# Performance work log

Hardware: AMD Instinct MI355X
Metric: run time of the kernel (lower is better)

## Reference

```python
import jax, jax.numpy as jnp
import numpy as np

N_NODES = 50000
N_PATHS = 4
N_EDGES = 800000
D_IN = 256
D_OUT = 256
D_HID = 128  # SemanticAttention default hidden_size


def setup_inputs() -> dict:
    key = jax.random.key(0)
    ks = jax.random.split(key, 6)
    x = jax.random.normal(ks[0], (N_NODES, D_IN), dtype=jnp.float32)
    edge_indices = jax.random.randint(ks[1], (N_PATHS, 2, N_EDGES), 0, N_NODES)
    Ws = jax.random.normal(ks[2], (N_PATHS, D_IN, D_OUT), dtype=jnp.float32) * (1.0 / np.sqrt(D_IN))
    bs = jnp.zeros((N_PATHS, D_OUT), dtype=jnp.float32)
    attn_w1 = jax.random.normal(ks[3], (D_OUT, D_HID), dtype=jnp.float32) * (1.0 / np.sqrt(D_OUT))
    attn_b1 = jnp.zeros((D_HID,), dtype=jnp.float32)
    attn_w2 = jax.random.normal(ks[4], (D_HID, 1), dtype=jnp.float32) * (1.0 / np.sqrt(D_HID))
    return {"x": x, "edge_indices": edge_indices, "Ws": Ws, "bs": bs,
            "attn_w1": attn_w1, "attn_b1": attn_b1, "attn_w2": attn_w2}


def _gcn_conv(x, W, b, edges):
    """PyG GCNConv with normalize=True, add_self_loops=True.
    out = D^{-1/2} (A + I) D^{-1/2} (x @ W) + b
    """
    n = x.shape[0]
    xw = x @ W  # [N, D_OUT]
    loop = jnp.arange(n, dtype=edges.dtype)
    src = jnp.concatenate([edges[0], loop])
    dst = jnp.concatenate([edges[1], loop])
    ones = jnp.ones(src.shape[0], dtype=x.dtype)
    deg = jax.ops.segment_sum(ones, dst, num_segments=n)  # in-degree incl. self loop
    dinv = jnp.where(deg > 0, jax.lax.rsqrt(deg), 0.0)
    norm = dinv[src] * dinv[dst]  # [E+N]
    msgs = xw[src] * norm[:, None]  # gather + scale
    return jax.ops.segment_sum(msgs, dst, num_segments=n) + b  # scatter-add


def reference(x, edge_indices, Ws, bs, attn_w1, attn_b1, attn_w2):
    P = edge_indices.shape[0]
    # per-meta-path GCN embeddings, stacked -> [N, P, D_OUT]
    z = jnp.stack([_gcn_conv(x, Ws[i], bs[i], edge_indices[i]) for i in range(P)], axis=1)
    # semantic attention: per-node softmax over meta-paths
    w = jnp.tanh(z @ attn_w1 + attn_b1) @ attn_w2  # [N, P, 1]
    beta = jax.nn.softmax(w, axis=1)
    return (beta * z).sum(axis=1)  # [N, D_OUT]
```

## Files before the change

kernel.cpp:

```cpp
#include <hip/hip_runtime.h>
#include <hip/hip_fp16.h>
#include <cstdint>
#include <cstddef>

#define NN 50000
#define NE 800000
#define NP 4
#define DD 256
#define HH 128
#define MPAD 50048
#define PADIDX 50000

#define NB 196
#define CAP 5120
#define SCAP 6144
#define EPB 4096
#define NBB ((NE + EPB - 1) / EPB)
#define BIN_BLOCKS (NBB * NP)

typedef _Float16 f16x8 __attribute__((ext_vector_type(8)));
typedef float f32x4 __attribute__((ext_vector_type(4)));
typedef unsigned short u16x8 __attribute__((ext_vector_type(8)));
typedef unsigned short u16x4 __attribute__((ext_vector_type(4)));

#define X_OCT (NN * DD / 8)
#define XP_OCT (MPAD * DD / 8)
#define W_OCT (NP * DD * DD / 8)
#define W1_OCT (HH * DD / 8)
#define CVT_BLOCKS ((XP_OCT + W_OCT + W1_OCT + 255) / 256)
#define GEMM_BLOCKS ((MPAD / 64) * NP)

__global__ __launch_bounds__(256) void k_bin(const int* __restrict__ edges,
                                             int* __restrict__ gcnt,
                                             unsigned int* __restrict__ binned,
                                             const float* __restrict__ x,
                                             const float* __restrict__ Ws,
                                             const float* __restrict__ w1,
                                             _Float16* __restrict__ xh,
                                             _Float16* __restrict__ Wt,
                                             _Float16* __restrict__ w1t) {
    const int bx = blockIdx.x;
    const int tid = threadIdx.x;
    if (bx < BIN_BLOCKS) {
        __shared__ int hist[256], lb[256], cur[256], gbase[256], wsum[4];
        __shared__ unsigned int stage[EPB];
        const int p  = bx / NBB;
        const int bc = bx - p * NBB;
        const int e0 = bc * EPB;
        const int total = min(EPB, NE - e0);
        const int* es = edges + (size_t)p * 2 * NE;
        const int* ed = es + NE;
        hist[tid] = 0;
        __syncthreads();
        unsigned int word[16];
        int bkt[16];
#pragma unroll
        for (int j = 0; j < 16; j++) {
            int e = e0 + j * 256 + tid;
            bkt[j] = -1;
            if (e < NE) {
                int dst = ed[e];
                int src = es[e];
                int b = dst >> 8;
                bkt[j] = b;
                word[j] = ((unsigned)b << 24) | ((unsigned)(dst & 255) << 16) | (unsigned)src;
                atomicAdd(&hist[b], 1);
            }
        }
        __syncthreads();
        const int lane = tid & 63, wv = tid >> 6;
        int v = hist[tid];
        int incl = v;
#pragma unroll
        for (int off = 1; off < 64; off <<= 1) {
            int u = __shfl_up(incl, off);
            if (lane >= off) incl += u;
        }
        if (lane == 63) wsum[wv] = incl;
        __syncthreads();
        int wbase = 0;
        for (int i = 0; i < wv; i++) wbase += wsum[i];
        int excl = wbase + incl - v;
        lb[tid] = excl;
        cur[tid] = excl;
        if (tid < NB && v > 0) gbase[tid] = atomicAdd(&gcnt[p * NB + tid], v);
        __syncthreads();
#pragma unroll
        for (int j = 0; j < 16; j++)
            if (bkt[j] >= 0) {
                int r = atomicAdd(&cur[bkt[j]], 1);
                stage[r] = word[j];
            }
        __syncthreads();
        for (int s = tid; s < total; s += 256) {
            unsigned int wd = stage[s];
            int b = wd >> 24;
            int posl = gbase[b] + (s - lb[b]);
            if (posl < CAP)
                binned[(size_t)(p * NB + b) * CAP + posl] = wd & 0x00FFFFFFu;
        }
        return;
    }
    int i = (bx - BIN_BLOCKS) * 256 + tid;
    if (i < XP_OCT) {
        f16x8 o;
        if (i < X_OCT) {
            const float4* src = (const float4*)x + (size_t)i * 2;
            float4 v0 = src[0], v1 = src[1];
            o[0] = (_Float16)v0.x; o[1] = (_Float16)v0.y; o[2] = (_Float16)v0.z; o[3] = (_Float16)v0.w;
            o[4] = (_Float16)v1.x; o[5] = (_Float16)v1.y; o[6] = (_Float16)v1.z; o[7] = (_Float16)v1.w;
        } else {
#pragma unroll
            for (int t = 0; t < 8; t++) o[t] = (_Float16)0.0f;
        }
        *((f16x8*)xh + i) = o;
    } else if (i < XP_OCT + W_OCT) {
        int j = i - XP_OCT;
        int p   = j / (DD * DD / 8);
        int rem = j - p * (DD * DD / 8);
        int n   = rem >> 5;
        int k8  = (rem & 31) * 8;
        const float* wp = Ws + (size_t)p * DD * DD;
        f16x8 o;
#pragma unroll
        for (int t = 0; t < 8; t++) o[t] = (_Float16)wp[(size_t)(k8 + t) * DD + n];
        *((f16x8*)(Wt + (size_t)p * DD * DD + (size_t)n * DD + k8)) = o;
    } else if (i < XP_OCT + W_OCT + W1_OCT) {
        int j = i - XP_OCT - W_OCT;
        int n  = j >> 5;
        int k8 = (j & 31) * 8;
        f16x8 o;
#pragma unroll
        for (int t = 0; t < 8; t++) o[t] = (_Float16)w1[(size_t)(k8 + t) * HH + n];
        *((f16x8*)(w1t + (size_t)n * DD + k8)) = o;
    }
}

__global__ __launch_bounds__(256) void k_sort(const int* __restrict__ gcnt,
                                              const unsigned int* __restrict__ binned,
                                              unsigned short* __restrict__ srcs,
                                              int* __restrict__ offs,
                                              int* __restrict__ ends,
                                              float* __restrict__ dinv) {
    __shared__ int hist[256], cur[256], wsum[4];
    __shared__ unsigned short sorted[SCAP];
    const int bx = blockIdx.x;
    const int tid = threadIdx.x;
    const int p = bx / NB, b = bx - p * NB;
    const int base = bx * SCAP;
    const int n = min(gcnt[bx], CAP);
    hist[tid] = 0;
#pragma unroll
    for (int j = 0; j < SCAP / 256; j++) sorted[j * 256 + tid] = (unsigned short)PADIDX;
    __syncthreads();
    unsigned int w[20];
#pragma unroll
    for (int j = 0; j < 20; j++) {
        int s = j * 256 + tid;
        w[j] = 0xFFFFFFFFu;
        if (s < n) {
            w[j] = binned[(size_t)bx * CAP + s];
            atomicAdd(&hist[(w[j] >> 16) & 255], 1);
        }
    }
    __syncthreads();
    const int lane = tid & 63, wv = tid >> 6;
    int v  = hist[tid];
    int pv = (v + 7) & ~7;
    int incl = pv;
#pragma unroll
    for (int off = 1; off < 64; off <<= 1) {
        int u = __shfl_up(incl, off);
        if (lane >= off) incl += u;
    }
    if (lane == 63) wsum[wv] = incl;
    __syncthreads();
    int wbase = 0;
    for (int i = 0; i < wv; i++) wbase += wsum[i];
    int excl = wbase + incl - pv;
    cur[tid] = excl;
    const int node = b * 256 + tid;
    if (node < NN) {
        int o = base + excl;
        offs[p * NN + node] = o;
        ends[p * NN + node] = o + pv;
        dinv[(size_t)p * MPAD + node] = rsqrtf((float)v + 1.0f);
    }
    __syncthreads();
    int totalpad = wsum[0] + wsum[1] + wsum[2] + wsum[3];
#pragma unroll
    for (int j = 0; j < 20; j++)
        if (w[j] != 0xFFFFFFFFu) {
            int r = atomicAdd(&cur[(w[j] >> 16) & 255], 1);
            if (r < SCAP) sorted[r] = (unsigned short)(w[j] & 0xFFFFu);
        }
    __syncthreads();
#pragma unroll
    for (int j = 0; j < SCAP / 256; j++) {
        int s = j * 256 + tid;
        if (s < totalpad && s < SCAP) srcs[base + s] = sorted[s];
    }
}

__global__ __launch_bounds__(256) void k_agg(const _Float16* __restrict__ xh,
                                             const float* __restrict__ dinv,
                                             const int* __restrict__ offs,
                                             const int* __restrict__ ends,
                                             const unsigned short* __restrict__ srcs,
                                             _Float16* __restrict__ agg) {
    const int wv = threadIdx.x >> 6;
    const int lane = threadIdx.x & 63;
    const int half = lane >> 5, hl = lane & 31;
    const int p = blockIdx.x / (NN / 4);
    const int n = (blockIdx.x - p * (NN / 4)) * 4 + wv;
    const float* dvp = dinv + (size_t)p * MPAD;

    const float dd = dvp[n];
    float facc[8];
    {
        f16x8 xv = *(const f16x8*)(xh + (size_t)n * DD + hl * 8);
#pragma unroll
        for (int t = 0; t < 8; t++) facc[t] = (half == 0) ? dd * (float)xv[t] : 0.0f;
    }

    int k  = offs[p * NN + n];
    int ke = ends[p * NN + n];
    for (; k + 16 <= ke; k += 16) {
        u16x8 su = *(const u16x8*)(srcs + k + half * 8);
        int s[8];
#pragma unroll
        for (int j = 0; j < 8; j++) s[j] = su[j];
        f16x8 v[8];
#pragma unroll
        for (int j = 0; j < 8; j++)
            v[j] = *(const f16x8*)(xh + (size_t)s[j] * DD + hl * 8);
        float dv[8];
#pragma unroll
        for (int j = 0; j < 8; j++) dv[j] = dvp[s[j]];
#pragma unroll
        for (int j = 0; j < 8; j++)
#pragma unroll
            for (int t = 0; t < 8; t++) facc[t] += dv[j] * (float)v[j][t];
    }
    if (k < ke) {
        u16x4 su = *(const u16x4*)(srcs + k + half * 4);
        int s[4];
#pragma unroll
        for (int j = 0; j < 4; j++) s[j] = su[j];
        f16x8 v[4];
#pragma unroll
        for (int j = 0; j < 4; j++)
            v[j] = *(const f16x8*)(xh + (size_t)s[j] * DD + hl * 8);
        float dv[4];
#pragma unroll
        for (int j = 0; j < 4; j++) dv[j] = dvp[s[j]];
#pragma unroll
        for (int j = 0; j < 4; j++)
#pragma unroll
            for (int t = 0; t < 8; t++) facc[t] += dv[j] * (float)v[j][t];
    }
#pragma unroll
    for (int t = 0; t < 8; t++) facc[t] += __shfl_xor(facc[t], 32);
    if (half == 0) {
        f16x8 o;
#pragma unroll
        for (int t = 0; t < 8; t++) o[t] = (_Float16)(dd * facc[t]);
        *(f16x8*)(agg + ((size_t)p * MPAD + n) * DD + hl * 8) = o;
    }
}

__global__ __launch_bounds__(256) void k_gemm(const _Float16* __restrict__ agg,
                                              const _Float16* __restrict__ Wt,
                                              const float* __restrict__ bs,
                                              _Float16* __restrict__ z) {
    const int gb   = blockIdx.x;
    const int p    = gb / (MPAD / 64);
    const int bm   = gb - p * (MPAD / 64);
    const int wv   = threadIdx.x >> 6;
    const int lane = threadIdx.x & 63;
    const int m_base = bm * 64;
    const int n0   = wv * 64;
    const int mr   = lane & 15;
    const int quad = lane >> 4;

    const _Float16* ap = agg + ((size_t)p * MPAD + m_base + mr) * DD + quad * 8;
    const _Float16* bp = Wt + (size_t)p * DD * DD + (size_t)(n0 + mr) * DD + quad * 8;
    _Float16* cp = z + (size_t)p * MPAD * DD;

    f32x4 acc[4][4] = {};
    for (int k0 = 0; k0 < DD; k0 += 32) {
        f16x8 a[4], b[4];
#pragma unroll
        for (int i = 0; i < 4; i++) a[i] = *(const f16x8*)(ap + (size_t)i * 16 * DD + k0);
#pragma unroll
        for (int j = 0; j < 4; j++) b[j] = *(const f16x8*)(bp + (size_t)j * 16 * DD + k0);
#pragma unroll
        for (int i = 0; i < 4; i++)
#pragma unroll
            for (int j = 0; j < 4; j++)
                acc[i][j] = __builtin_amdgcn_mfma_f32_16x16x32_f16(a[i], b[j], acc[i][j], 0, 0, 0);
    }
    float bb[4];
#pragma unroll
    for (int j = 0; j < 4; j++) bb[j] = bs[p * DD + n0 + j * 16 + mr];
#pragma unroll
    for (int i = 0; i < 4; i++) {
#pragma unroll
        for (int r = 0; r < 4; r++) {
            int row = m_base + i * 16 + quad * 4 + r;
#pragma unroll
            for (int j = 0; j < 4; j++)
                cp[(size_t)row * DD + n0 + j * 16 + mr] = (_Float16)(acc[i][j][r] + bb[j]);
        }
    }
}

__global__ __launch_bounds__(512) void k_attn(const _Float16* __restrict__ z,
                                              const _Float16* __restrict__ w1t,
                                              const float* __restrict__ b1,
                                              const float* __restrict__ w2,
                                              float* __restrict__ out) {
    const int tid  = threadIdx.x;
    const int w    = tid >> 6;
    const int lane = tid & 63;
    const int quad = lane >> 4, mr = lane & 15;

    __shared__ __align__(16) _Float16 zs[64][264];
    __shared__ __align__(16) _Float16 w1s[128][264];

    const int n0 = blockIdx.x * 16;

#pragma unroll
    for (int j = 0; j < 8; j++) {
        int o = j * 512 + tid;
        int r = o >> 5, oc = o & 31;
        *(f16x8*)&w1s[r][oc * 8] = *(const f16x8*)(w1t + (size_t)r * DD + oc * 8);
    }
#pragma unroll
    for (int j = 0; j < 4; j++) {
        int o = j * 512 + tid;
        int r = o >> 5, oc = o & 31;
        int nl = r >> 2, p = r & 3;
        *(f16x8*)&zs[r][oc * 8] = *(const f16x8*)(z + ((size_t)p * MPAD + n0 + nl) * DD + oc * 8);
    }
    __syncthreads();
    if (w >= 4) return;

    f32x4 acch[8] = {};
    for (int k0 = 0; k0 < DD; k0 += 32) {
        f16x8 a = *(const f16x8*)&zs[w * 16 + mr][k0 + quad * 8];
#pragma unroll
        for (int j = 0; j < 8; j++) {
            f16x8 b = *(const f16x8*)&w1s[j * 16 + mr][k0 + quad * 8];
            acch[j] = __builtin_amdgcn_mfma_f32_16x16x32_f16(a, b, acch[j], 0, 0, 0);
        }
    }

    float part[4] = {};
#pragma unroll
    for (int j = 0; j < 8; j++) {
        int col = j * 16 + mr;
        float bb = b1[col], ww = w2[col];
#pragma unroll
        for (int r = 0; r < 4; r++)
            part[r] += tanhf(acch[j][r] + bb) * ww;
    }
#pragma unroll
    for (int off = 1; off < 16; off <<= 1) {
#pragma unroll
        for (int r = 0; r < 4; r++) part[r] += __shfl_xor(part[r], off);
    }
    float m = fmaxf(fmaxf(part[0], part[1]), fmaxf(part[2], part[3]));
    float e0 = __expf(part[0] - m), e1 = __expf(part[1] - m),
          e2 = __expf(part[2] - m), e3 = __expf(part[3] - m);
    float rr = 1.0f / (e0 + e1 + e2 + e3);
    float be[4] = {e0 * rr, e1 * rr, e2 * rr, e3 * rr};

    const int n  = blockIdx.x * 16 + w * 4 + quad;
    const int rb = w * 16 + quad * 4;
    float o[16] = {};
#pragma unroll
    for (int p = 0; p < 4; p++) {
        f16x8 z0 = *(const f16x8*)&zs[rb + p][mr * 16];
        f16x8 z1 = *(const f16x8*)&zs[rb + p][mr * 16 + 8];
#pragma unroll
        for (int t = 0; t < 8; t++) {
            o[t]     += be[p] * (float)z0[t];
            o[t + 8] += be[p] * (float)z1[t];
        }
    }
#pragma unroll
    for (int t = 0; t < 16; t += 4)
        *(float4*)(out + (size_t)n * DD + mr * 16 + t) =
            make_float4(o[t], o[t + 1], o[t + 2], o[t + 3]);
}

extern "C" void kernel_launch(void* const* d_in, const int* in_sizes, int n_in,
                              void* d_out, int out_size, void* d_ws, size_t ws_size,
                              hipStream_t stream) {
    const float* x     = (const float*)d_in[0];
    const int*   edges = (const int*)d_in[1];
    const float* Ws    = (const float*)d_in[2];
    const float* bs    = (const float*)d_in[3];
    const float* w1    = (const float*)d_in[4];
    const float* b1    = (const float*)d_in[5];
    const float* w2    = (const float*)d_in[6];
    float* out = (float*)d_out;

    char* ws = (char*)d_ws;
    _Float16*       agg    = (_Float16*)ws;
    _Float16*       Wt     = (_Float16*)(ws + (98 << 20));
    _Float16*       w1t    = (_Float16*)(ws + (98 << 20) + (1 << 19));
    _Float16*       z      = (_Float16*)(ws + (104 << 20));
    _Float16*       xh     = (_Float16*)(ws + (104 << 20));
    unsigned int*   binned = (unsigned int*)(ws + (130 << 20));
    unsigned short* srcs   = (unsigned short*)(ws + (147 << 20));
    float*          dinv   = (float*)(ws + (157 << 20));
    int*            offs   = (int*)(ws + (158 << 20));
    int*            ends   = (int*)(ws + (159 << 20));
    int*            gcnt   = (int*)(ws + (160 << 20));

    hipMemsetAsync(gcnt, 0, NP * NB * sizeof(int), stream);
    hipMemsetAsync(dinv, 0, (size_t)NP * MPAD * sizeof(float), stream);

    k_bin<<<BIN_BLOCKS + CVT_BLOCKS, 256, 0, stream>>>(
        edges, gcnt, binned, x, Ws, w1, xh, Wt, w1t);

    k_sort<<<NP * NB, 256, 0, stream>>>(gcnt, binned, srcs, offs, ends, dinv);

    k_agg<<<NP * NN / 4, 256, 0, stream>>>(xh, dinv, offs, ends, srcs, agg);

    k_gemm<<<GEMM_BLOCKS, 256, 0, stream>>>(agg, Wt, bs, z);

    k_attn<<<NN / 16, 512, 0, stream>>>(z, w1t, b1, w2, out);
}
```

Measured before the change: 555.2 us.

## Fuse sparse aggregation into GEMM via LDS tile; widen attention blocks

Sparse aggregation and the per-path GEMM now run in one kernel. Each block aggregates 64 node rows into shared memory and then multiplies them by W directly, so the fp16 agg intermediate is never written to or read back from global memory. The attention kernel now handles 32 nodes per block with all 8 waves doing MFMA work. It reads w1 from global/L2 instead of staging it in LDS. The tradeoff is far fewer aggregation blocks (sequential loops of 16 nodes per wave), which lowers parallelism and the ability to hide latency in the gather-bound phase.

```diff
diff --git a/kernel.cpp b/kernel.cpp
--- a/kernel.cpp
+++ b/kernel.cpp
@@ -28,7 +28,8 @@
 #define W_OCT (NP * DD * DD / 8)
 #define W1_OCT (HH * DD / 8)
 #define CVT_BLOCKS ((XP_OCT + W_OCT + W1_OCT + 255) / 256)
-#define GEMM_BLOCKS ((MPAD / 64) * NP)
+#define GA_BLOCKS ((MPAD / 64) * NP)
+#define AT_BLOCKS ((NN + 31) / 32)
 
 __global__ __launch_bounds__(256) void k_bin(const int* __restrict__ edges,
                                              int* __restrict__ gcnt,
@@ -202,88 +203,87 @@
     }
 }
 
-__global__ __launch_bounds__(256) void k_agg(const _Float16* __restrict__ xh,
-                                             const float* __restrict__ dinv,
-                                             const int* __restrict__ offs,
-                                             const int* __restrict__ ends,
-                                             const unsigned short* __restrict__ srcs,
-                                             _Float16* __restrict__ agg) {
-    const int wv = threadIdx.x >> 6;
-    const int lane = threadIdx.x & 63;
-    const int half = lane >> 5, hl = lane & 31;
-    const int p = blockIdx.x / (NN / 4);
-    const int n = (blockIdx.x - p * (NN / 4)) * 4 + wv;
-    const float* dvp = dinv + (size_t)p * MPAD;
-
-    const float dd = dvp[n];
-    float facc[8];
-    {
-        f16x8 xv = *(const f16x8*)(xh + (size_t)n * DD + hl * 8);
-#pragma unroll
-        for (int t = 0; t < 8; t++) facc[t] = (half == 0) ? dd * (float)xv[t] : 0.0f;
-    }
-
-    int k  = offs[p * NN + n];
-    int ke = ends[p * NN + n];
-    for (; k + 16 <= ke; k += 16) {
-        u16x8 su = *(const u16x8*)(srcs + k + half * 8);
-        int s[8];
-#pragma unroll
-        for (int j = 0; j < 8; j++) s[j] = su[j];
-        f16x8 v[8];
-#pragma unroll
-        for (int j = 0; j < 8; j++)
-            v[j] = *(const f16x8*)(xh + (size_t)s[j] * DD + hl * 8);
-        float dv[8];
-#pragma unroll
-        for (int j = 0; j < 8; j++) dv[j] = dvp[s[j]];
-#pragma unroll
-        for (int j = 0; j < 8; j++)
-#pragma unroll
-            for (int t = 0; t < 8; t++) facc[t] += dv[j] * (float)v[j][t];
-    }
-    if (k < ke) {
-        u16x4 su = *(const u16x4*)(srcs + k + half * 4);
-        int s[4];
-#pragma unroll
-        for (int j = 0; j < 4; j++) s[j] = su[j];
-        f16x8 v[4];
-#pragma unroll
-        for (int j = 0; j < 4; j++)
-            v[j] = *(const f16x8*)(xh + (size_t)s[j] * DD + hl * 8);
-        float dv[4];
-#pragma unroll
-        for (int j = 0; j < 4; j++) dv[j] = dvp[s[j]];
-#pragma unroll
-        for (int j = 0; j < 4; j++)
-#pragma unroll
-            for (int t = 0; t < 8; t++) facc[t] += dv[j] * (float)v[j][t];
-    }
-#pragma unroll
-    for (int t = 0; t < 8; t++) facc[t] += __shfl_xor(facc[t], 32);
-    if (half == 0) {
-        f16x8 o;
-#pragma unroll
-        for (int t = 0; t < 8; t++) o[t] = (_Float16)(dd * facc[t]);
-        *(f16x8*)(agg + ((size_t)p * MPAD + n) * DD + hl * 8) = o;
-    }
-}
-
-__global__ __launch_bounds__(256) void k_gemm(const _Float16* __restrict__ agg,
-                                              const _Float16* __restrict__ Wt,
-                                              const float* __restrict__ bs,
-                                              _Float16* __restrict__ z) {
+__global__ __launch_bounds__(256) void k_gemmagg(const _Float16* __restrict__ xh,
+                                                 const float* __restrict__ dinv,
+                                                 const int* __restrict__ offs,
+                                                 const int* __restrict__ ends,
+                                                 const unsigned short* __restrict__ srcs,
+                                                 const _Float16* __restrict__ Wt,
+                                                 const float* __restrict__ bs,
+                                                 _Float16* __restrict__ z) {
     const int gb   = blockIdx.x;
     const int p    = gb / (MPAD / 64);
     const int bm   = gb - p * (MPAD / 64);
+    const int m_base = bm * 64;
     const int wv   = threadIdx.x >> 6;
     const int lane = threadIdx.x & 63;
-    const int m_base = bm * 64;
-    const int n0   = wv * 64;
-    const int mr   = lane & 15;
-    const int quad = lane >> 4;
-
-    const _Float16* ap = agg + ((size_t)p * MPAD + m_base + mr) * DD + quad * 8;
+    const int half = lane >> 5, hl = lane & 31;
+    const int mr   = lane & 15, quad = lane >> 4;
+
+    __shared__ __align__(16) _Float16 as[64][264];
+
+    const float* dvp = dinv + (size_t)p * MPAD;
+
+#pragma unroll 1
+    for (int q = 0; q < 16; q++) {
+        const int n = m_base + wv * 16 + q;
+        const float dd = dvp[n];
+        float facc[8];
+        {
+            f16x8 xv = *(const f16x8*)(xh + (size_t)n * DD + hl * 8);
+#pragma unroll
+            for (int t = 0; t < 8; t++) facc[t] = (half == 0) ? dd * (float)xv[t] : 0.0f;
+        }
+        if (n < NN) {
+            int k  = offs[p * NN + n];
+            int ke = ends[p * NN + n];
+            for (; k + 16 <= ke; k += 16) {
+                u16x8 su = *(const u16x8*)(srcs + k + half * 8);
+                int s[8];
+#pragma unroll
+                for (int j = 0; j < 8; j++) s[j] = su[j];
+                f16x8 v[8];
+#pragma unroll
+                for (int j = 0; j < 8; j++)
+                    v[j] = *(const f16x8*)(xh + (size_t)s[j] * DD + hl * 8);
+                float dv[8];
+#pragma unroll
+                for (int j = 0; j < 8; j++) dv[j] = dvp[s[j]];
+#pragma unroll
+                for (int j = 0; j < 8; j++)
+#pragma unroll
+                    for (int t = 0; t < 8; t++) facc[t] += dv[j] * (float)v[j][t];
+            }
+            if (k < ke) {
+                u16x4 su = *(const u16x4*)(srcs + k + half * 4);
+                int s[4];
+#pragma unroll
+                for (int j = 0; j < 4; j++) s[j] = su[j];
+                f16x8 v[4];
+#pragma unroll
+                for (int j = 0; j < 4; j++)
+                    v[j] = *(const f16x8*)(xh + (size_t)s[j] * DD + hl * 8);
+                float dv[4];
+#pragma unroll
+                for (int j = 0; j < 4; j++) dv[j] = dvp[s[j]];
+#pragma unroll
+                for (int j = 0; j < 4; j++)
+#pragma unroll
+                    for (int t = 0; t < 8; t++) facc[t] += dv[j] * (float)v[j][t];
+            }
+        }
+#pragma unroll
+        for (int t = 0; t < 8; t++) facc[t] += __shfl_xor(facc[t], 32);
+        if (half == 0) {
+            f16x8 o;
+#pragma unroll
+            for (int t = 0; t < 8; t++) o[t] = (_Float16)(dd * facc[t]);
+            *(f16x8*)&as[wv * 16 + q][hl * 8] = o;
+        }
+    }
+    __syncthreads();
+
+    const int n0 = wv * 64;
     const _Float16* bp = Wt + (size_t)p * DD * DD + (size_t)(n0 + mr) * DD + quad * 8;
     _Float16* cp = z + (size_t)p * MPAD * DD;
 
@@ -291,7 +291,7 @@
     for (int k0 = 0; k0 < DD; k0 += 32) {
         f16x8 a[4], b[4];
 #pragma unroll
-        for (int i = 0; i < 4; i++) a[i] = *(const f16x8*)(ap + (size_t)i * 16 * DD + k0);
+        for (int i = 0; i < 4; i++) a[i] = *(const f16x8*)&as[i * 16 + mr][k0 + quad * 8];
 #pragma unroll
         for (int j = 0; j < 4; j++) b[j] = *(const f16x8*)(bp + (size_t)j * 16 * DD + k0);
 #pragma unroll
@@ -325,33 +325,26 @@
     const int lane = tid & 63;
     const int quad = lane >> 4, mr = lane & 15;
 
-    __shared__ __align__(16) _Float16 zs[64][264];
-    __shared__ __align__(16) _Float16 w1s[128][264];
-
-    const int n0 = blockIdx.x * 16;
+    __shared__ __align__(16) _Float16 zs[128][264];
+
+    const int nb = blockIdx.x * 32;
 
 #pragma unroll
     for (int j = 0; j < 8; j++) {
         int o = j * 512 + tid;
         int r = o >> 5, oc = o & 31;
-        *(f16x8*)&w1s[r][oc * 8] = *(const f16x8*)(w1t + (size_t)r * DD + oc * 8);
-    }
-#pragma unroll
-    for (int j = 0; j < 4; j++) {
-        int o = j * 512 + tid;
-        int r = o >> 5, oc = o & 31;
         int nl = r >> 2, p = r & 3;
-        *(f16x8*)&zs[r][oc * 8] = *(const f16x8*)(z + ((size_t)p * MPAD + n0 + nl) * DD + oc * 8);
-    }
-    __syncthreads();
-    if (w >= 4) return;
+        *(f16x8*)&zs[r][oc * 8] =
+            *(const f16x8*)(z + ((size_t)p * MPAD + nb + nl) * DD + oc * 8);
+    }
+    __syncthreads();
 
     f32x4 acch[8] = {};
     for (int k0 = 0; k0 < DD; k0 += 32) {
         f16x8 a = *(const f16x8*)&zs[w * 16 + mr][k0 + quad * 8];
 #pragma unroll
         for (int j = 0; j < 8; j++) {
-            f16x8 b = *(const f16x8*)&w1s[j * 16 + mr][k0 + quad * 8];
+            f16x8 b = *(const f16x8*)(w1t + (size_t)(j * 16 + mr) * DD + k0 + quad * 8);
             acch[j] = __builtin_amdgcn_mfma_f32_16x16x32_f16(a, b, acch[j], 0, 0, 0);
         }
     }
@@ -376,7 +369,7 @@
     float rr = 1.0f / (e0 + e1 + e2 + e3);
     float be[4] = {e0 * rr, e1 * rr, e2 * rr, e3 * rr};
 
-    const int n  = blockIdx.x * 16 + w * 4 + quad;
+    const int n  = nb + w * 4 + quad;
     const int rb = w * 16 + quad * 4;
     float o[16] = {};
 #pragma unroll
@@ -389,10 +382,12 @@
             o[t + 8] += be[p] * (float)z1[t];
         }
     }
-#pragma unroll
-    for (int t = 0; t < 16; t += 4)
-        *(float4*)(out + (size_t)n * DD + mr * 16 + t) =
-            make_float4(o[t], o[t + 1], o[t + 2], o[t + 3]);
+    if (n < NN) {
+#pragma unroll
+        for (int t = 0; t < 16; t += 4)
+            *(float4*)(out + (size_t)n * DD + mr * 16 + t) =
+                make_float4(o[t], o[t + 1], o[t + 2], o[t + 3]);
+    }
 }
 
 extern "C" void kernel_launch(void* const* d_in, const int* in_sizes, int n_in,
@@ -408,17 +403,16 @@
     float* out = (float*)d_out;
 
     char* ws = (char*)d_ws;
-    _Float16*       agg    = (_Float16*)ws;
-    _Float16*       Wt     = (_Float16*)(ws + (98 << 20));
-    _Float16*       w1t    = (_Float16*)(ws + (98 << 20) + (1 << 19));
-    _Float16*       z      = (_Float16*)(ws + (104 << 20));
-    _Float16*       xh     = (_Float16*)(ws + (104 << 20));
-    unsigned int*   binned = (unsigned int*)(ws + (130 << 20));
-    unsigned short* srcs   = (unsigned short*)(ws + (147 << 20));
-    float*          dinv   = (float*)(ws + (157 << 20));
-    int*            offs   = (int*)(ws + (158 << 20));
-    int*            ends   = (int*)(ws + (159 << 20));
-    int*            gcnt   = (int*)(ws + (160 << 20));
+    _Float16*       xh     = (_Float16*)ws;
+    _Float16*       Wt     = (_Float16*)(ws + (26 << 20));
+    _Float16*       w1t    = (_Float16*)(ws + (26 << 20) + (1 << 19));
+    float*          dinv   = (float*)(ws + (27 << 20));
+    int*            offs   = (int*)(ws + (28 << 20));
+    int*            ends   = (int*)(ws + (29 << 20));
+    unsigned short* srcs   = (unsigned short*)(ws + (30 << 20));
+    unsigned int*   binned = (unsigned int*)(ws + (40 << 20));
+    int*            gcnt   = (int*)(ws + (57 << 20));
+    _Float16*       z      = (_Float16*)(ws + (58 << 20));
 
     hipMemsetAsync(gcnt, 0, NP * NB * sizeof(int), stream);
     hipMemsetAsync(dinv, 0, (size_t)NP * MPAD * sizeof(float), stream);
@@ -428,9 +422,7 @@
 
     k_sort<<<NP * NB, 256, 0, stream>>>(gcnt, binned, srcs, offs, ends, dinv);
 
-    k_agg<<<NP * NN / 4, 256, 0, stream>>>(xh, dinv, offs, ends, srcs, agg);
-
-    k_gemm<<<GEMM_BLOCKS, 256, 0, stream>>>(agg, Wt, bs, z);
-
-    k_attn<<<NN / 16, 512, 0, stream>>>(z, w1t, b1, w2, out);
+    k_gemmagg<<<GA_BLOCKS, 256, 0, stream>>>(xh, dinv, offs, ends, srcs, Wt, bs, z);
+
+    k_attn<<<AT_BLOCKS, 512, 0, stream>>>(z, w1t, b1, w2, out);
 }
```

New measurement: 592.7 us. 1.07x slower.
